# Performance work log

Hardware: AMD Instinct MI355X
Metric: run time of the kernel (lower is better)

The kernel has to match this reference:

```python
import jax, jax.numpy as jnp
import numpy as np

B, N, NV = 2, 4096, 32768
HID = 128
XD, YD, ZD = 128, 128, 16  # dense occupancy grid dims (original derives from coord maxima)


def setup_inputs() -> dict:
    key = jax.random.key(0)
    ks = jax.random.split(key, 12)
    position = jax.random.normal(ks[0], (B, N, 3), jnp.float32) * 20.0
    scale = jax.random.uniform(ks[1], (B, N, 3), jnp.float32)
    rotation = jax.random.normal(ks[2], (B, N, 4), jnp.float32)
    opacity = jax.random.uniform(ks[3], (B, N, 1), jnp.float32)
    # sparse voxel coords: [batch_idx, x, y, z]
    b_idx = jax.random.randint(ks[4], (NV, 1), 0, B)
    xs = jax.random.randint(ks[5], (NV, 1), 0, XD)
    ys = jax.random.randint(ks[6], (NV, 1), 0, YD)
    zs = jax.random.randint(ks[7], (NV, 1), 0, ZD)
    voxel_coords = jnp.concatenate([b_idx, xs, ys, zs], axis=1).astype(jnp.int32)
    # MLP params: Linear(11,128) -> ReLU -> Linear(128,128)
    W1 = jax.random.normal(ks[8], (11, HID), jnp.float32) * (1.0 / np.sqrt(11))
    b1 = jnp.zeros((HID,), jnp.float32)
    W2 = jax.random.normal(ks[9], (HID, HID), jnp.float32) * (1.0 / np.sqrt(HID))
    b2 = jnp.zeros((HID,), jnp.float32)
    return {"position": position, "scale": scale, "rotation": rotation,
            "opacity": opacity, "W1": W1, "b1": b1, "W2": W2, "b2": b2,
            "voxel_coords": voxel_coords}


def reference(position, scale, rotation, opacity, W1, b1, W2, b2, voxel_coords):
    # concat gaussian attributes -> (B, N, 11)
    x = jnp.concatenate([position, scale, rotation, opacity], axis=-1)
    x = jnp.maximum(x @ W1 + b1, 0.0) @ W2 + b2  # (B, N, HID)

    # anchor grid: linspace(-50,50, N^(1/3))^3 -> (N, 3)
    n_side = int(round(N ** (1.0 / 3.0)))
    anchor_pos = jnp.linspace(-50.0, 50.0, n_side)
    grid = jnp.stack(jnp.meshgrid(anchor_pos, anchor_pos, anchor_pos, indexing="ij"), axis=-1)
    anchor_grid = grid.reshape(-1, 3)  # (N, 3)

    batch_ids = voxel_coords[:, 0]
    xyz = voxel_coords[:, 1:].astype(jnp.float32)  # (NV, 3)

    # Euclidean cdist (NV, N) via ||a||^2 + ||b||^2 - 2ab
    d2 = (jnp.sum(xyz * xyz, axis=1, keepdims=True)
          + jnp.sum(anchor_grid * anchor_grid, axis=1)[None, :]
          - 2.0 * (xyz @ anchor_grid.T))
    dist = jnp.sqrt(jnp.maximum(d2, 0.0))
    weight = jax.nn.softmax(-dist, axis=-1)  # (NV, N)

    fused = jnp.einsum("vn,bnd->bvd", weight, x)  # (B, NV, HID)

    # scatter into dense 5D occupancy grid (vectorized over all batches)
    occ = jnp.zeros((B, HID, XD, YD, ZD), jnp.float32)
    vals = fused[batch_ids, jnp.arange(NV)]  # (NV, HID) per-voxel feature from its own batch
    occ = occ.at[batch_ids, :, voxel_coords[:, 1], voxel_coords[:, 2], voxel_coords[:, 3]].set(vals)
    return occ
```

## Files before the change

### kernel.cpp

```cpp
#include <hip/hip_runtime.h>
#include <hip/hip_bf16.h>

#define B_    2
#define N_    4096
#define NV_   32768
#define HID_  128
#define XD_   128
#define YD_   128
#define ZD_   16
#define PLANE (XD_*YD_*ZD_)
#define LOCS  (B_*PLANE)
#define STEP  (100.0f/15.0f)
#define NT    64
#define VB    64

typedef __attribute__((ext_vector_type(8))) short short8;
typedef __attribute__((ext_vector_type(4))) float f32x4;

__device__ __forceinline__ float anchor_coord(int i) {
    return fmaf((float)i, STEP, -50.0f);
}
__device__ __forceinline__ unsigned short f2bf(float x) {
    unsigned u = __float_as_uint(x);
    return (unsigned short)((u + 0x7fffu + ((u >> 16) & 1u)) >> 16);
}

__global__ __launch_bounds__(256) void mlp_kernel(
    const float* __restrict__ pos, const float* __restrict__ scl,
    const float* __restrict__ rot, const float* __restrict__ opa,
    const float* __restrict__ W1,  const float* __restrict__ b1,
    const float* __restrict__ W2,  const float* __restrict__ b2,
    unsigned short* __restrict__ xwT)
{
    int rg = threadIdx.x >> 7;
    int j  = threadIdx.x & 127;
    int r  = blockIdx.x * 2 + rg;
    __shared__ float sin_[2][11];
    __shared__ float h[2][HID_];
    if (j < 11) {
        float val;
        if (j < 3)       val = pos[r*3 + j];
        else if (j < 6)  val = scl[r*3 + (j-3)];
        else if (j < 10) val = rot[r*4 + (j-6)];
        else             val = opa[r];
        sin_[rg][j] = val;
    }
    __syncthreads();
    float a = b1[j];
    #pragma unroll
    for (int i = 0; i < 11; ++i) a = fmaf(sin_[rg][i], W1[i*HID_ + j], a);
    h[rg][j] = fmaxf(a, 0.0f);
    __syncthreads();
    float o = b2[j];
    for (int k = 0; k < HID_; ++k) o = fmaf(h[rg][k], W2[k*HID_ + j], o);
    int b = r >> 12, n = r & 4095;
    xwT[((size_t)(b*HID_ + j))*N_ + n] = f2bf(o);
}

__global__ __launch_bounds__(256) void scatter_kernel(
    const int* __restrict__ vc, int* __restrict__ map,
    int* __restrict__ cnt, int* __restrict__ vlist)
{
    int v = blockIdx.x * 256 + threadIdx.x;
    int4 c = ((const int4*)vc)[v];
    int loc = ((c.x*XD_ + c.y)*YD_ + c.z)*ZD_ + c.w;
    atomicMax(&map[loc], v);
    int lane = threadIdx.x & 63;
    unsigned long long m1 = __ballot(c.x != 0);
    unsigned long long mymask = c.x ? m1 : ~m1;
    int leader = (int)__ffsll(mymask) - 1;
    int total  = __popcll(mymask);
    int rank   = __popcll(mymask & ((1ull << lane) - 1ull));
    int base = 0;
    if (lane == leader) base = atomicAdd(&cnt[c.x], total);
    base = __shfl(base, leader);
    vlist[c.x*NV_ + base + rank] = v;
}

__global__ __launch_bounds__(256) void ml_kernel(
    const int* __restrict__ vc, float2* __restrict__ ml)
{
    int gid = blockIdx.x * 256 + threadIdx.x;
    int v = gid >> 3, sub = gid & 7;
    int4 c = ((const int4*)vc)[v];
    float vx = (float)c.y, vy = (float)c.z, vz = (float)c.w;
    float dz2_[16];
    #pragma unroll 16
    for (int iz = 0; iz < 16; ++iz) { float t = vz - anchor_coord(iz); dz2_[iz] = t*t; }

    float m = 1e30f, l = 0.0f;
    #pragma unroll
    for (int i = 0; i < 2; ++i) {
        float dx = vx - anchor_coord(sub*2 + i);
        float dx2 = dx*dx;
        for (int iy = 0; iy < 16; ++iy) {
            float dy = vy - anchor_coord(iy);
            float bxy = fmaf(dy, dy, dx2);
            #pragma unroll 16
            for (int iz = 0; iz < 16; ++iz) {
                float d = sqrtf(bxy + dz2_[iz]);
                float dm = d - m;
                float e = __expf(-fabsf(dm));
                bool nm = dm < 0.0f;
                l = nm ? fmaf(l, e, 1.0f) : (l + e);
                m = nm ? d : m;
            }
        }
    }
    #pragma unroll
    for (int off = 1; off < 8; off <<= 1) {
        float m2 = __shfl_xor(m, off);
        float l2 = __shfl_xor(l, off);
        float mn = fminf(m, m2);
        l = l * __expf(mn - m) + l2 * __expf(mn - m2);
        m = mn;
    }
    if (sub == 0) ml[v] = make_float2(m, 1.0f / l);
}

__global__ __launch_bounds__(256) void fuse_kernel(
    const unsigned short* __restrict__ xwT, const float2* __restrict__ ml,
    const int* __restrict__ vc,   const int* __restrict__ vlist,
    const int* __restrict__ cnt,  float* __restrict__ fused)
{
    int seg = blockIdx.x >> 9;
    int bi  = blockIdx.x & 511;
    int count = cnt[seg];
    int vbase = bi * VB;
    if (vbase >= count) return;
    int nv = min(VB, count - vbase);

    __shared__ uint4 sXT[128*8];
    __shared__ uint4 sP [64*8];
    __shared__ float svx[VB], svy[VB], svz[VB], sdm[VB], sil[VB];
    __shared__ int   svid[VB];

    int tid = threadIdx.x;
    if (tid < VB) {
        int vid = -1; float fx=0, fy=0, fz=0, dm=0, il=0;
        if (tid < nv) {
            vid = vlist[seg*NV_ + vbase + tid];
            int4 c = ((const int4*)vc)[vid];
            fx = (float)c.y; fy = (float)c.z; fz = (float)c.w;
            float2 t = ml[vid]; dm = t.x; il = t.y;
        }
        svid[tid]=vid; svx[tid]=fx; svy[tid]=fy; svz[tid]=fz; sdm[tid]=dm; sil[tid]=il;
    }
    __syncthreads();

    int pv = tid & 63, png = tid >> 6;
    float pvx = svx[pv], pvy = svy[pv], pvz = svz[pv];
    float pdm = sdm[pv], pil = sil[pv];
    float dz2_[16];
    #pragma unroll 16
    for (int iz = 0; iz < 16; ++iz) { float t = pvz - anchor_coord(iz); dz2_[iz] = t*t; }

    int wv = tid >> 6, L = tid & 63;
    int wr = wv >> 1, wc = wv & 1;
    int r  = L & 15,  g  = L >> 4;
    f32x4 acc[2][4];
    #pragma unroll
    for (int i = 0; i < 2; ++i)
        #pragma unroll
        for (int jj = 0; jj < 4; ++jj) acc[i][jj] = (f32x4){0.f,0.f,0.f,0.f};

    int sd = tid >> 1, ss = tid & 1;
    const uint4* xg = (const uint4*)xwT + ((size_t)(seg*128 + sd) * N_ >> 3);

    for (int t = 0; t < N_/NT; ++t) {
        int n0 = t * NT;
        __syncthreads();
        {
            const uint4* src = xg + (n0 >> 3) + ss*4;
            int dbase = sd * 8;
            #pragma unroll
            for (int i = 0; i < 4; ++i) {
                int blk = ss*4 + i;
                sXT[dbase + (blk ^ (sd & 7))] = src[i];
            }
        }
        {
            int nc = n0 + png*16;
            int idx = nc >> 4;
            float ax = anchor_coord(idx >> 4);
            float ay = anchor_coord(idx & 15);
            float dxv = pvx - ax, dyv = pvy - ay;
            float bxy = fmaf(dxv, dxv, dyv*dyv);
            unsigned u[8];
            #pragma unroll
            for (int jj = 0; jj < 8; ++jj) {
                float d0 = sqrtf(bxy + dz2_[2*jj]);
                float d1 = sqrtf(bxy + dz2_[2*jj+1]);
                float p0 = __expf(pdm - d0) * pil;
                float p1 = __expf(pdm - d1) * pil;
                asm("v_cvt_pk_bf16_f32 %0, %1, %2" : "=v"(u[jj]) : "v"(p0), "v"(p1));
            }
            int pb = pv * 8;
            sP[pb + ((png*2    ) ^ (pv & 7))] = make_uint4(u[0],u[1],u[2],u[3]);
            sP[pb + ((png*2 + 1) ^ (pv & 7))] = make_uint4(u[4],u[5],u[6],u[7]);
        }
        __syncthreads();
        #pragma unroll
        for (int ks = 0; ks < 2; ++ks) {
            int blk = ks*4 + g;
            int va0 = wr*32 + r;
            int va1 = va0 + 16;
            short8 a0 = *(const short8*)&sP[va0*8 + (blk ^ (va0 & 7))];
            short8 a1 = *(const short8*)&sP[va1*8 + (blk ^ (va1 & 7))];
            #pragma unroll
            for (int df = 0; df < 4; ++df) {
                int dr = wc*64 + df*16 + r;
                short8 bb = *(const short8*)&sXT[dr*8 + (blk ^ (dr & 7))];
                acc[0][df] = __builtin_amdgcn_mfma_f32_16x16x32_bf16(a0, bb, acc[0][df], 0, 0, 0);
                acc[1][df] = __builtin_amdgcn_mfma_f32_16x16x32_bf16(a1, bb, acc[1][df], 0, 0, 0);
            }
        }
    }

    #pragma unroll
    for (int vi = 0; vi < 2; ++vi)
        #pragma unroll
        for (int df = 0; df < 4; ++df)
            #pragma unroll
            for (int q = 0; q < 4; ++q) {
                int vloc = wr*32 + vi*16 + g*4 + q;
                int dcol = wc*64 + df*16 + r;
                if (vloc < nv) {
                    fused[(size_t)svid[vloc]*HID_ + dcol] = acc[vi][df][q];
                }
            }
}

__global__ __launch_bounds__(256) void out_kernel(
    const int* __restrict__ map, const float* __restrict__ fused,
    float* __restrict__ out)
{
    int loc = blockIdx.x * 256 + threadIdx.x;
    int b   = loc >> 18;
    int rem = loc & (PLANE - 1);
    int v   = map[loc];
    const float* frow = fused + (size_t)(v < 0 ? 0 : v) * HID_;
    size_t obase = ((size_t)b * HID_) * PLANE + rem;
    for (int ch = 0; ch < HID_; ++ch) {
        float val = 0.0f;
        if (v >= 0) val = frow[ch];
        out[obase + (size_t)ch * PLANE] = val;
    }
}

extern "C" void kernel_launch(void* const* d_in, const int* in_sizes, int n_in,
                              void* d_out, int out_size, void* d_ws, size_t ws_size,
                              hipStream_t stream) {
    const float* pos = (const float*)d_in[0];
    const float* scl = (const float*)d_in[1];
    const float* rot = (const float*)d_in[2];
    const float* opa = (const float*)d_in[3];
    const float* W1  = (const float*)d_in[4];
    const float* b1  = (const float*)d_in[5];
    const float* W2  = (const float*)d_in[6];
    const float* b2  = (const float*)d_in[7];
    const int*   vc  = (const int*)d_in[8];
    float* out = (float*)d_out;

    char* ws = (char*)d_ws;
    unsigned short* xwT = (unsigned short*)(ws);
    float2* ml    = (float2*)(ws + (2u<<20));
    float*  fused = (float*) (ws + (4u<<20));
    int*    map   = (int*)   (ws + (20u<<20));
    int*    vlist = (int*)   (ws + (22u<<20));
    int*    cnt   = (int*)   (ws + (23u<<20));

    hipMemsetAsync(map, 0xFF, LOCS*sizeof(int), stream);
    hipMemsetAsync(cnt, 0, 2*sizeof(int), stream);

    mlp_kernel<<<(B_*N_)/2, 256, 0, stream>>>(pos, scl, rot, opa, W1, b1, W2, b2, xwT);
    scatter_kernel<<<NV_/256, 256, 0, stream>>>(vc, map, cnt, vlist);
    ml_kernel<<<(NV_*8)/256, 256, 0, stream>>>(vc, ml);
    fuse_kernel<<<2*512, 256, 0, stream>>>(xwT, ml, vc, vlist, cnt, fused);
    out_kernel<<<LOCS/256, 256, 0, stream>>>(map, fused, out);
}
```

Baseline: 319.6 us.

## Split-K fuse kernel with atomics, base-2 exp scaling, vectorized output writes

Splits the fuse kernel's reduction over anchors into four chunks, launching four times as many blocks. Partial results are accumulated into a zero-initialised fused buffer with atomic adds, and the 1/l normalisation is applied at the end. Coordinates are prescaled by log2(e) so the raw v_exp_f32 instruction replaces __expf. The output kernel now handles four locations per thread and writes float4 stores. These changes raise occupancy and cut instruction count and store transactions, at the cost of an extra memset and atomic traffic.

```diff
diff --git a/kernel.cpp b/kernel.cpp
--- a/kernel.cpp
+++ b/kernel.cpp
@@ -13,12 +13,20 @@
 #define STEP  (100.0f/15.0f)
 #define NT    64
 #define VB    64
+#define KS    4
+#define L2E   1.4426950408889634f
 
 typedef __attribute__((ext_vector_type(8))) short short8;
 typedef __attribute__((ext_vector_type(4))) float f32x4;
 
 __device__ __forceinline__ float anchor_coord(int i) {
     return fmaf((float)i, STEP, -50.0f);
+}
+__device__ __forceinline__ float anchor_s(int i) {
+    return fmaf((float)i, STEP * L2E, -50.0f * L2E);
+}
+__device__ __forceinline__ float fexp2(float x) {
+    float r; asm("v_exp_f32 %0, %1" : "=v"(r) : "v"(x)); return r;
 }
 __device__ __forceinline__ unsigned short f2bf(float x) {
     unsigned u = __float_as_uint(x);
@@ -83,24 +91,24 @@
     int gid = blockIdx.x * 256 + threadIdx.x;
     int v = gid >> 3, sub = gid & 7;
     int4 c = ((const int4*)vc)[v];
-    float vx = (float)c.y, vy = (float)c.z, vz = (float)c.w;
+    float vx = (float)c.y * L2E, vy = (float)c.z * L2E, vz = (float)c.w * L2E;
     float dz2_[16];
     #pragma unroll 16
-    for (int iz = 0; iz < 16; ++iz) { float t = vz - anchor_coord(iz); dz2_[iz] = t*t; }
+    for (int iz = 0; iz < 16; ++iz) { float t = vz - anchor_s(iz); dz2_[iz] = t*t; }
 
     float m = 1e30f, l = 0.0f;
     #pragma unroll
     for (int i = 0; i < 2; ++i) {
-        float dx = vx - anchor_coord(sub*2 + i);
+        float dx = vx - anchor_s(sub*2 + i);
         float dx2 = dx*dx;
         for (int iy = 0; iy < 16; ++iy) {
-            float dy = vy - anchor_coord(iy);
+            float dy = vy - anchor_s(iy);
             float bxy = fmaf(dy, dy, dx2);
             #pragma unroll 16
             for (int iz = 0; iz < 16; ++iz) {
                 float d = sqrtf(bxy + dz2_[iz]);
                 float dm = d - m;
-                float e = __expf(-fabsf(dm));
+                float e = fexp2(-fabsf(dm));
                 bool nm = dm < 0.0f;
                 l = nm ? fmaf(l, e, 1.0f) : (l + e);
                 m = nm ? d : m;
@@ -112,7 +120,7 @@
         float m2 = __shfl_xor(m, off);
         float l2 = __shfl_xor(l, off);
         float mn = fminf(m, m2);
-        l = l * __expf(mn - m) + l2 * __expf(mn - m2);
+        l = l * fexp2(mn - m) + l2 * fexp2(mn - m2);
         m = mn;
     }
     if (sub == 0) ml[v] = make_float2(m, 1.0f / l);
@@ -123,12 +131,16 @@
     const int* __restrict__ vc,   const int* __restrict__ vlist,
     const int* __restrict__ cnt,  float* __restrict__ fused)
 {
-    int seg = blockIdx.x >> 9;
-    int bi  = blockIdx.x & 511;
+    int bid = blockIdx.x;
+    int ks_ = bid & (KS-1);
+    int rest = bid >> 2;
+    int seg = rest >> 9;
+    int bi  = rest & 511;
     int count = cnt[seg];
     int vbase = bi * VB;
     if (vbase >= count) return;
     int nv = min(VB, count - vbase);
+    int k0 = ks_ * (N_/KS);
 
     __shared__ uint4 sXT[128*8];
     __shared__ uint4 sP [64*8];
@@ -141,7 +153,7 @@
         if (tid < nv) {
             vid = vlist[seg*NV_ + vbase + tid];
             int4 c = ((const int4*)vc)[vid];
-            fx = (float)c.y; fy = (float)c.z; fz = (float)c.w;
+            fx = (float)c.y * L2E; fy = (float)c.z * L2E; fz = (float)c.w * L2E;
             float2 t = ml[vid]; dm = t.x; il = t.y;
         }
         svid[tid]=vid; svx[tid]=fx; svy[tid]=fy; svz[tid]=fz; sdm[tid]=dm; sil[tid]=il;
@@ -150,10 +162,10 @@
 
     int pv = tid & 63, png = tid >> 6;
     float pvx = svx[pv], pvy = svy[pv], pvz = svz[pv];
-    float pdm = sdm[pv], pil = sil[pv];
+    float pml = sdm[pv];
     float dz2_[16];
     #pragma unroll 16
-    for (int iz = 0; iz < 16; ++iz) { float t = pvz - anchor_coord(iz); dz2_[iz] = t*t; }
+    for (int iz = 0; iz < 16; ++iz) { float t = pvz - anchor_s(iz); dz2_[iz] = t*t; }
 
     int wv = tid >> 6, L = tid & 63;
     int wr = wv >> 1, wc = wv & 1;
@@ -167,8 +179,8 @@
     int sd = tid >> 1, ss = tid & 1;
     const uint4* xg = (const uint4*)xwT + ((size_t)(seg*128 + sd) * N_ >> 3);
 
-    for (int t = 0; t < N_/NT; ++t) {
-        int n0 = t * NT;
+    for (int t = 0; t < (N_/KS)/NT; ++t) {
+        int n0 = k0 + t * NT;
         __syncthreads();
         {
             const uint4* src = xg + (n0 >> 3) + ss*4;
@@ -182,8 +194,8 @@
         {
             int nc = n0 + png*16;
             int idx = nc >> 4;
-            float ax = anchor_coord(idx >> 4);
-            float ay = anchor_coord(idx & 15);
+            float ax = anchor_s(idx >> 4);
+            float ay = anchor_s(idx & 15);
             float dxv = pvx - ax, dyv = pvy - ay;
             float bxy = fmaf(dxv, dxv, dyv*dyv);
             unsigned u[8];
@@ -191,8 +203,8 @@
             for (int jj = 0; jj < 8; ++jj) {
                 float d0 = sqrtf(bxy + dz2_[2*jj]);
                 float d1 = sqrtf(bxy + dz2_[2*jj+1]);
-                float p0 = __expf(pdm - d0) * pil;
-                float p1 = __expf(pdm - d1) * pil;
+                float p0 = fexp2(pml - d0);
+                float p1 = fexp2(pml - d1);
                 asm("v_cvt_pk_bf16_f32 %0, %1, %2" : "=v"(u[jj]) : "v"(p0), "v"(p1));
             }
             int pb = pv * 8;
@@ -201,8 +213,8 @@
         }
         __syncthreads();
         #pragma unroll
-        for (int ks = 0; ks < 2; ++ks) {
-            int blk = ks*4 + g;
+        for (int kss = 0; kss < 2; ++kss) {
+            int blk = kss*4 + g;
             int va0 = wr*32 + r;
             int va1 = va0 + 16;
             short8 a0 = *(const short8*)&sP[va0*8 + (blk ^ (va0 & 7))];
@@ -226,7 +238,8 @@
                 int vloc = wr*32 + vi*16 + g*4 + q;
                 int dcol = wc*64 + df*16 + r;
                 if (vloc < nv) {
-                    fused[(size_t)svid[vloc]*HID_ + dcol] = acc[vi][df][q];
+                    atomicAdd(&fused[(size_t)svid[vloc]*HID_ + dcol],
+                              acc[vi][df][q] * sil[vloc]);
                 }
             }
 }
@@ -235,16 +248,27 @@
     const int* __restrict__ map, const float* __restrict__ fused,
     float* __restrict__ out)
 {
-    int loc = blockIdx.x * 256 + threadIdx.x;
-    int b   = loc >> 18;
-    int rem = loc & (PLANE - 1);
-    int v   = map[loc];
-    const float* frow = fused + (size_t)(v < 0 ? 0 : v) * HID_;
+    int q = blockIdx.x * 256 + threadIdx.x;
+    int loc0 = q << 2;
+    int b   = loc0 >> 18;
+    int rem = loc0 & (PLANE - 1);
+    int4 vv = ((const int4*)map)[q];
+    const float4* r0 = (const float4*)(fused + (size_t)(vv.x < 0 ? 0 : vv.x) * HID_);
+    const float4* r1 = (const float4*)(fused + (size_t)(vv.y < 0 ? 0 : vv.y) * HID_);
+    const float4* r2 = (const float4*)(fused + (size_t)(vv.z < 0 ? 0 : vv.z) * HID_);
+    const float4* r3 = (const float4*)(fused + (size_t)(vv.w < 0 ? 0 : vv.w) * HID_);
     size_t obase = ((size_t)b * HID_) * PLANE + rem;
-    for (int ch = 0; ch < HID_; ++ch) {
-        float val = 0.0f;
-        if (v >= 0) val = frow[ch];
-        out[obase + (size_t)ch * PLANE] = val;
+    const float4 z4 = make_float4(0.f, 0.f, 0.f, 0.f);
+    #pragma unroll 4
+    for (int chb = 0; chb < 32; ++chb) {
+        float4 a = (vv.x >= 0) ? r0[chb] : z4;
+        float4 c = (vv.y >= 0) ? r1[chb] : z4;
+        float4 d = (vv.z >= 0) ? r2[chb] : z4;
+        float4 e = (vv.w >= 0) ? r3[chb] : z4;
+        *(float4*)&out[obase + (size_t)(chb*4 + 0) * PLANE] = make_float4(a.x, c.x, d.x, e.x);
+        *(float4*)&out[obase + (size_t)(chb*4 + 1) * PLANE] = make_float4(a.y, c.y, d.y, e.y);
+        *(float4*)&out[obase + (size_t)(chb*4 + 2) * PLANE] = make_float4(a.z, c.z, d.z, e.z);
+        *(float4*)&out[obase + (size_t)(chb*4 + 3) * PLANE] = make_float4(a.w, c.w, d.w, e.w);
     }
 }
 
@@ -272,10 +296,11 @@
 
     hipMemsetAsync(map, 0xFF, LOCS*sizeof(int), stream);
     hipMemsetAsync(cnt, 0, 2*sizeof(int), stream);
+    hipMemsetAsync(fused, 0, (size_t)NV_*HID_*sizeof(float), stream);
 
     mlp_kernel<<<(B_*N_)/2, 256, 0, stream>>>(pos, scl, rot, opa, W1, b1, W2, b2, xwT);
     scatter_kernel<<<NV_/256, 256, 0, stream>>>(vc, map, cnt, vlist);
     ml_kernel<<<(NV_*8)/256, 256, 0, stream>>>(vc, ml);
-    fuse_kernel<<<2*512, 256, 0, stream>>>(xwT, ml, vc, vlist, cnt, fused);
-    out_kernel<<<LOCS/256, 256, 0, stream>>>(map, fused, out);
-}
+    fuse_kernel<<<2*512*KS, 256, 0, stream>>>(xwT, ml, vc, vlist, cnt, fused);
+    out_kernel<<<LOCS/(256*4), 256, 0, stream>>>(map, fused, out);
+}
```

Measured after the change: 283.2 us. -11.4%, faster.
